# Optimization experiments

Measured on AMD Instinct MI355X. Metric: run time of the kernel, lower is better.

The kernel has to match this reference:

```python
import jax, jax.numpy as jnp
import numpy as np

BANDWIDTH = 0.1
N_STEPS = 5
TOL = 1e-3
BASE = 3
COORD_OFFSET = 512   # bins assumed within (-512, 511] per dim
COORD_BITS = 10      # 3 dims * 10 bits = 30 bits, fits int32


def _generate_offsets(d, base=3):
    # replicates torch.meshgrid(indexing='ij') over arange(-1, base-1)
    ranges = [np.arange(-1, base - 1) for _ in range(d)]
    mesh = np.meshgrid(*ranges, indexing='ij')
    return jnp.asarray(np.stack(mesh, axis=-1).reshape(-1, d), dtype=jnp.int32)


def _pack_keys(bins):
    # bins: (..., d) int32 -> unique scalar int32 key per bin coordinate
    d = bins.shape[-1]
    key = jnp.zeros(bins.shape[:-1], dtype=jnp.int32)
    for k in range(d):  # tiny fixed loop over dims
        key = (key << COORD_BITS) | (bins[..., k] + COORD_OFFSET)
    return key


def _step(X, offsets, bandwidth):
    # One mean-shift step: bin points, scatter-add sums/counts over the
    # union of offset-shifted bins (torch.unique replaced by exact key
    # packing + sort-based grouping, fixed shapes for jit).
    n, d = X.shape
    m = offsets.shape[0]  # base ** d
    bins = (X / bandwidth).astype(jnp.int32)          # trunc-toward-zero == torch .int()
    shifted = bins[:, None, :] + offsets[None, :, :]  # (n, m, d)
    keys = _pack_keys(shifted).reshape(-1)            # (n*m,)
    K = keys.shape[0]

    order = jnp.argsort(keys)
    skeys = keys[order]
    new_grp = jnp.concatenate(
        [jnp.zeros((1,), jnp.int32), (skeys[1:] != skeys[:-1]).astype(jnp.int32)]
    )
    seg = jnp.cumsum(new_grp)                         # group id per sorted position

    # X repeated once per offset (matches X.repeat(1, m).reshape(-1, d))
    Xflat = jnp.broadcast_to(X[:, None, :], (n, m, d)).reshape(-1, d)
    sum_per = jax.ops.segment_sum(Xflat[order], seg, num_segments=K)          # (K, d)
    cnt_per = jax.ops.segment_sum(jnp.ones((K,), X.dtype), seg, num_segments=K)

    # segment id per original (unsorted) flat position == inverse_indices
    seg_orig = jnp.zeros((K,), seg.dtype).at[order].set(seg)
    sum_mapped = sum_per[seg_orig].reshape(n, m, d).sum(axis=1)   # (n, d)
    cnt_mapped = cnt_per[seg_orig].reshape(n, m).sum(axis=1)      # (n,)
    return sum_mapped / cnt_mapped[:, None]


def setup_inputs() -> dict:
    key = jax.random.key(0)
    X = jax.random.normal(key, (200000, 3), dtype=jnp.float32)
    return {"X": X}


def reference(X):
    n, d = X.shape
    offsets = _generate_offsets(d, BASE)

    def body(carry, _):
        Xc, done = carry
        Xn = _step(Xc, offsets, BANDWIDTH)
        Xn = jnp.where(done, Xc, Xn)  # freeze once converged (== early break)
        conv = jnp.max(jnp.linalg.norm(Xn - Xc, axis=1)) <= TOL
        return (Xn, done | conv), None

    (Xout, _), _ = jax.lax.scan(body, (X, jnp.array(False)), None, length=N_STEPS)
    return Xout
```

## Files before the change

### kernel.cpp

```cpp
#include <hip/hip_runtime.h>


constexpr float BW   = 0.1f;
constexpr float TOL2 = 1e-6f;
constexpr int DIM  = 112, OFF = 56;
constexpr int DIM2 = DIM * DIM;
constexpr int CELLS = DIM * DIM * DIM;
constexpr int CLW = CELLS / 32;
constexpr int RDIM = 16, RC = 7;
constexpr int NREG = RDIM * RDIM * RDIM;
constexpr int RC3 = RC * RC * RC;
constexpr int NB_A = 128, BLK = 256;
constexpr int NF = 2048;
constexpr int IPB = 51;
constexpr float FPS = 16777216.0f;
constexpr double FPSI = 1.0 / 16777216.0;

typedef float vf2 __attribute__((ext_vector_type(2)));

__device__ __forceinline__ int clampb(int v) { return v < 0 ? 0 : (v > DIM - 1 ? DIM - 1 : v); }
__device__ __forceinline__ int binf(float v) { return clampb((int)(v / BW) + OFF); }
__device__ __forceinline__ int flatb(int bx, int by, int bz) { return (bx * DIM + by) * DIM + bz; }
__device__ __forceinline__ int regOf(int bx, int by, int bz) {
    return ((bx / RC) * RDIM + (by / RC)) * RDIM + (bz / RC);
}
__device__ __forceinline__ int lcOf(int bx, int by, int bz) {
    return ((bx % RC) * RC + (by % RC)) * RC + (bz % RC);
}

__device__ __forceinline__ void pk_add(float* p, float a, float b) {
#if defined(__has_builtin) && __has_builtin(__builtin_amdgcn_global_atomic_fadd_v2f32)
    vf2 v = {a, b};
    __builtin_amdgcn_global_atomic_fadd_v2f32((vf2*)p, v);
#else
    atomicAdd(p, a);
    atomicAdd(p + 1, b);
#endif
}

__launch_bounds__(BLK)
__global__ void k_histA(const float* __restrict__ X, int n, int* __restrict__ blockHist,
                        float4* __restrict__ zeroB) {
    __shared__ int h[NREG];
    for (int i = threadIdx.x; i < NREG; i += blockDim.x) h[i] = 0;
    __syncthreads();
    int stride = gridDim.x * blockDim.x;
    for (int i = blockIdx.x * blockDim.x + threadIdx.x; i < n; i += stride) {
        float x = X[3 * i + 0], y = X[3 * i + 1], z = X[3 * i + 2];
        atomicAdd(&h[regOf(binf(x), binf(y), binf(z))], 1);
    }
    __syncthreads();
    for (int i = threadIdx.x; i < NREG; i += blockDim.x)
        blockHist[blockIdx.x * NREG + i] = h[i];
    for (int i = blockIdx.x * blockDim.x + threadIdx.x; i < CELLS; i += stride)
        zeroB[i] = make_float4(0.f, 0.f, 0.f, 0.f);
}

__global__ void k_colscan(int* __restrict__ blockHist, int* __restrict__ regionPS) {
    int r = blockIdx.x * blockDim.x + threadIdx.x;
    if (r >= NREG) return;
    int run = 0;
    for (int b = 0; b < NB_A; ++b) {
        int idx = b * NREG + r;
        int v = blockHist[idx];
        blockHist[idx] = run;
        run += v;
    }
    regionPS[r] = run;
}

__launch_bounds__(1024)
__global__ void k_regprefix(int* __restrict__ regionPS) {
    __shared__ int buf[1024];
    int t = threadIdx.x;
    int v0 = regionPS[4 * t + 0], v1 = regionPS[4 * t + 1];
    int v2 = regionPS[4 * t + 2], v3 = regionPS[4 * t + 3];
    int s = v0 + v1 + v2 + v3;
    buf[t] = s;
    __syncthreads();
    for (int d = 1; d < 1024; d <<= 1) {
        int add = (t >= d) ? buf[t - d] : 0;
        __syncthreads();
        buf[t] += add;
        __syncthreads();
    }
    int excl = buf[t] - s;
    regionPS[4 * t + 0] = excl;
    regionPS[4 * t + 1] = excl + v0;
    regionPS[4 * t + 2] = excl + v0 + v1;
    regionPS[4 * t + 3] = excl + v0 + v1 + v2;
    if (t == 1023) regionPS[4096] = buf[1023];
}

__launch_bounds__(BLK)
__global__ void k_scatterA(const float* __restrict__ X, int n,
                           const int* __restrict__ blockHist,
                           const int* __restrict__ regionPS,
                           float4* __restrict__ bucket, float4* __restrict__ zeroC) {
    __shared__ int cur[NREG];
    for (int i = threadIdx.x; i < NREG; i += blockDim.x) cur[i] = 0;
    __syncthreads();
    int stride = gridDim.x * blockDim.x;
    for (int i = blockIdx.x * blockDim.x + threadIdx.x; i < n; i += stride) {
        float x = X[3 * i + 0], y = X[3 * i + 1], z = X[3 * i + 2];
        int r = regOf(binf(x), binf(y), binf(z));
        int pos = regionPS[r] + blockHist[blockIdx.x * NREG + r] + atomicAdd(&cur[r], 1);
        bucket[pos] = make_float4(x, y, z, __int_as_float(i));
    }
    for (int i = blockIdx.x * blockDim.x + threadIdx.x; i < CELLS; i += stride)
        zeroC[i] = make_float4(0.f, 0.f, 0.f, 0.f);
}

__launch_bounds__(BLK)
__global__ void k_binB(const float4* __restrict__ bucket, const int* __restrict__ regionPS,
                       float4* __restrict__ A, int* __restrict__ E0,
                       int* __restrict__ PIdx, int* __restrict__ gM0) {
    __shared__ unsigned long long aX[RC3], aY[RC3], aZ[RC3];
    __shared__ unsigned aC[RC3];
    __shared__ int cidx[RC3];
    __shared__ int cnt, cur, sBase;
    int r = blockIdx.x;
    for (int c = threadIdx.x; c < RC3; c += blockDim.x) {
        aX[c] = 0ull; aY[c] = 0ull; aZ[c] = 0ull; aC[c] = 0u;
    }
    if (threadIdx.x == 0) { cnt = 0; cur = 0; }
    __syncthreads();
    int start = regionPS[r], end = regionPS[r + 1];
    for (int i = start + threadIdx.x; i < end; i += blockDim.x) {
        float4 p = bucket[i];
        int lc = lcOf(binf(p.x), binf(p.y), binf(p.z));
        atomicAdd(&aX[lc], (unsigned long long)(long long)rintf(p.x * FPS));
        atomicAdd(&aY[lc], (unsigned long long)(long long)rintf(p.y * FPS));
        atomicAdd(&aZ[lc], (unsigned long long)(long long)rintf(p.z * FPS));
        atomicAdd(&aC[lc], 1u);
    }
    __syncthreads();
    int myc = 0;
    for (int c = threadIdx.x; c < RC3; c += blockDim.x)
        if (aC[c] > 0u) ++myc;
    if (myc) atomicAdd(&cnt, myc);
    __syncthreads();
    if (threadIdx.x == 0 && cnt > 0) sBase = atomicAdd(gM0, cnt);
    __syncthreads();
    int rx = r / (RDIM * RDIM), ry = (r / RDIM) % RDIM, rz = r % RDIM;
    for (int c = threadIdx.x; c < RC3; c += blockDim.x) {
        if (aC[c] > 0u) {
            int idx = sBase + atomicAdd(&cur, 1);
            cidx[c] = idx;
            int bx = rx * RC + c / (RC * RC);
            int by = ry * RC + (c / RC) % RC;
            int bz = rz * RC + c % RC;
            int b = flatb(bx, by, bz);
            E0[idx] = b;
            A[b] = make_float4((float)((double)(long long)aX[c] * FPSI),
                               (float)((double)(long long)aY[c] * FPSI),
                               (float)((double)(long long)aZ[c] * FPSI),
                               (float)aC[c]);
        }
    }
    __syncthreads();
    for (int i = start + threadIdx.x; i < end; i += blockDim.x) {
        float4 p = bucket[i];
        int lc = lcOf(binf(p.x), binf(p.y), binf(p.z));
        PIdx[__float_as_int(p.w)] = cidx[lc];
    }
}

__launch_bounds__(BLK)
__global__ void k_compactM(unsigned* __restrict__ mask, int* __restrict__ listOut,
                           int* __restrict__ pKout) {
    __shared__ int scan[BLK];
    __shared__ int sBase;
    int i = blockIdx.x * blockDim.x + threadIdx.x;
    unsigned w = (i < CLW) ? mask[i] : 0u;
    if (i < CLW && w) mask[i] = 0u;
    int c = __popc(w);
    scan[threadIdx.x] = c;
    __syncthreads();
    for (int d = 1; d < BLK; d <<= 1) {
        int add = (threadIdx.x >= (unsigned)d) ? scan[threadIdx.x - d] : 0;
        __syncthreads();
        scan[threadIdx.x] += add;
        __syncthreads();
    }
    if (threadIdx.x == BLK - 1) {
        int tot = scan[BLK - 1];
        sBase = tot ? atomicAdd(pKout, tot) : 0;
    }
    __syncthreads();
    int base = sBase + scan[threadIdx.x] - c;
    int bb = i * 32;
    while (w) {
        int b = __ffs(w) - 1;
        listOut[base++] = bb + b;
        w &= w - 1;
    }
}

__launch_bounds__(BLK)
__global__ void k_fused(
    const float4* __restrict__ src, const int* __restrict__ list, const int* __restrict__ pK,
    float4* __restrict__ REo, int* __restrict__ IDXo, float4* __restrict__ eposInit,
    float4* __restrict__ tgt, unsigned* __restrict__ clT,
    int updS, const float* __restrict__ X, int n, const int* __restrict__ PIdx,
    const float4* __restrict__ REp, const int* __restrict__ IDXp,
    const int* __restrict__ pM0, float4* __restrict__ epos,
    unsigned* __restrict__ notConv,
    const int* __restrict__ clearList, const int* __restrict__ pKc,
    float4* __restrict__ clearGrid, int lastStep) {
    __shared__ float4 sh[BLK];
    __shared__ unsigned sFlag;
    if (threadIdx.x == 0) sFlag = 0;
    __syncthreads();
    int K = *pK;
    int BC = (K + IPB - 1) / IPB;
    if (BC > NF - 256) BC = NF - 256;
    const float t5[5] = {1.f, 2.f, 3.f, 2.f, 1.f};
    bool moved = false;

    if ((int)blockIdx.x < BC) {
        for (int ib = blockIdx.x; ib * IPB < K; ib += BC) {
            int li = threadIdx.x / 5;
            int dx = threadIdx.x % 5;
            int item = ib * IPB + li;
            float4 part = make_float4(0.f, 0.f, 0.f, 0.f);
            if (li < IPB && item < K) {
                int b = list[item];
                int bx = b / DIM2, rem = b % DIM2;
                int by = rem / DIM, bz = rem % DIM;
                int ix = bx + dx - 2;
                if ((unsigned)ix < (unsigned)DIM) {
                    float wx = t5[dx];
                    if (by >= 2 && by <= DIM - 3 && bz >= 2 && bz <= DIM - 3) {
                        #pragma unroll
                        for (int dy = 0; dy < 5; ++dy) {
                            float wxy = wx * t5[dy];
                            const float4* row = src + flatb(ix, by + dy - 2, bz - 2);
                            #pragma unroll
                            for (int dz = 0; dz < 5; ++dz) {
                                float w = wxy * t5[dz];
                                float4 e = row[dz];
                                part.x = fmaf(w, e.x, part.x);
                                part.y = fmaf(w, e.y, part.y);
                                part.z = fmaf(w, e.z, part.z);
                                part.w = fmaf(w, e.w, part.w);
                            }
                        }
                    } else {
                        for (int dy = 0; dy < 5; ++dy) {
                            int iy = by + dy - 2;
                            if ((unsigned)iy >= (unsigned)DIM) continue;
                            float wxy = wx * t5[dy];
                            for (int dz = 0; dz < 5; ++dz) {
                                int iz = bz + dz - 2;
                                if ((unsigned)iz >= (unsigned)DIM) continue;
                                float w = wxy * t5[dz];
                                float4 e = src[flatb(ix, iy, iz)];
                                part.x = fmaf(w, e.x, part.x);
                                part.y = fmaf(w, e.y, part.y);
                                part.z = fmaf(w, e.z, part.z);
                                part.w = fmaf(w, e.w, part.w);
                            }
                        }
                    }
                }
            }
            sh[threadIdx.x] = part;
            __syncthreads();
            if (threadIdx.x < IPB) {
                int item2 = ib * IPB + threadIdx.x;
                if (item2 < K) {
                    int base5 = threadIdx.x * 5;
                    float4 a0 = sh[base5 + 0], a1 = sh[base5 + 1], a2 = sh[base5 + 2];
                    float4 a3 = sh[base5 + 3], a4 = sh[base5 + 4];
                    float sx = a0.x + a1.x + a2.x + a3.x + a4.x;
                    float sy = a0.y + a1.y + a2.y + a3.y + a4.y;
                    float sz = a0.z + a1.z + a2.z + a3.z + a4.z;
                    float sc = a0.w + a1.w + a2.w + a3.w + a4.w;
                    int b = list[item2];
                    float W = src[b].w;
                    float4 np = make_float4(sx / sc, sy / sc, sz / sc, W);
                    REo[item2] = np;
                    IDXo[b] = item2;
                    if (eposInit) eposInit[item2] = np;
                    if (!lastStep) {
                        int bn = flatb(binf(np.x), binf(np.y), binf(np.z));
                        float* cell = (float*)&tgt[bn];
                        pk_add(cell + 0, W * np.x, W * np.y);
                        pk_add(cell + 2, W * np.z, W);
                        atomicOr(&clT[(unsigned)bn >> 5], 1u << (bn & 31));
                    }
                }
            }
            __syncthreads();
        }
    } else {
        int U = (updS > 0) ? (X ? n : *pM0) : 0;
        int CL = clearList ? *pKc : 0;
        int total = U + CL;
        bool done = false;
        if (updS > 1) {
            for (int t = 1; t < updS; ++t) done |= (notConv[t] == 0u);
        }
        int stride = (NF - BC) * blockDim.x;
        for (int idx = (blockIdx.x - BC) * blockDim.x + threadIdx.x; idx < total;
             idx += stride) {
            if (idx < U) {
                int e = idx;
                if (X) {
                    float x = X[3 * e + 0], y = X[3 * e + 1], z = X[3 * e + 2];
                    float4 rr = REp[PIdx[e]];
                    float ex = rr.x - x, ey = rr.y - y, ez = rr.z - z;
                    moved |= (fmaf(ex, ex, fmaf(ey, ey, ez * ez)) > TOL2);
                } else if (!done) {
                    float4 p = epos[e];
                    int j = IDXp[flatb(binf(p.x), binf(p.y), binf(p.z))];
                    float4 rr = REp[j];
                    float ex = rr.x - p.x, ey = rr.y - p.y, ez = rr.z - p.z;
                    moved |= (fmaf(ex, ex, fmaf(ey, ey, ez * ez)) > TOL2);
                    epos[e] = make_float4(rr.x, rr.y, rr.z, p.w);
                }
            } else {
                clearGrid[clearList[idx - U]] = make_float4(0.f, 0.f, 0.f, 0.f);
            }
        }
    }
    if (moved) sFlag = 1;
    __syncthreads();
    if (threadIdx.x == 0 && updS > 0 && sFlag) notConv[updS] = 1u;
}

__launch_bounds__(BLK)
__global__ void k_fin(const float4* __restrict__ REa, const int* __restrict__ IDXa,
                      const float4* __restrict__ epos, const int* __restrict__ pM0,
                      const unsigned* __restrict__ notConv, float4* __restrict__ fpos) {
    int M0 = *pM0;
    bool done = false;
    for (int t = 1; t <= 4; ++t) done |= (notConv[t] == 0u);
    for (int e = blockIdx.x * blockDim.x + threadIdx.x; e < M0;
         e += gridDim.x * blockDim.x) {
        float4 p = epos[e];
        if (!done) {
            float4 rr = REa[IDXa[flatb(binf(p.x), binf(p.y), binf(p.z))]];
            p.x = rr.x; p.y = rr.y; p.z = rr.z;
        }
        fpos[e] = p;
    }
}

__global__ void k_map(const int* __restrict__ PIdx, int n, const float4* __restrict__ fpos,
                      float* __restrict__ out) {
    int i = blockIdx.x * blockDim.x + threadIdx.x;
    if (i >= n) return;
    float4 p = fpos[PIdx[i]];
    out[3 * i + 0] = p.x;
    out[3 * i + 1] = p.y;
    out[3 * i + 2] = p.z;
}

extern "C" void kernel_launch(void* const* d_in, const int* in_sizes, int n_in,
                              void* d_out, int out_size, void* d_ws, size_t ws_size,
                              hipStream_t stream) {
    const float* X = (const float*)d_in[0];
    int n = in_sizes[0] / 3;

    char* ws = (char*)d_ws;
    int*      cnt     = (int*)ws;
    unsigned* notConv = (unsigned*)(ws + 32);
    size_t mB = (size_t)CLW * 4;
    size_t gB = (size_t)CELLS * 16;
    unsigned* m0 = (unsigned*)(ws + 256);
    unsigned* m1 = (unsigned*)(ws + 256 + mB);
    float4* A = (float4*)(ws + 256 + 2 * mB);
    float4* B = (float4*)((char*)A + gB);
    float4* C = (float4*)((char*)B + gB);
    int* IDXa = (int*)((char*)C + gB);
    int* IDXb = IDXa + CELLS;
    float4* REa  = (float4*)(IDXb + CELLS);
    float4* REb  = REa + n;
    float4* epos = REb + n;
    int* E0   = (int*)(epos + n);
    int* La   = E0 + n;
    int* Lb   = La + n;
    int* Lc   = Lb + n;
    int* Ld   = Lc + n;
    int* PIdx = Ld + n;
    float4* bucket = (float4*)(PIdx + n);
    int* blockHist = (int*)(bucket + n);
    int* regionPS  = blockHist + NB_A * NREG;

    hipMemsetAsync(ws, 0, 256 + 2 * mB + gB, stream);

    const int NCM = (CLW + BLK - 1) / BLK;

    k_histA<<<NB_A, BLK, 0, stream>>>(X, n, blockHist, B);
    k_colscan<<<NREG / BLK, BLK, 0, stream>>>(blockHist, regionPS);
    k_regprefix<<<1, 1024, 0, stream>>>(regionPS);
    k_scatterA<<<NB_A, BLK, 0, stream>>>(X, n, blockHist, regionPS, bucket, C);
    k_binB<<<NREG, BLK, 0, stream>>>(bucket, regionPS, A, E0, PIdx, &cnt[1]);

    k_fused<<<NF, BLK, 0, stream>>>(A, E0, &cnt[1], REa, IDXa, epos,
                                    B, m0,
                                    0, nullptr, n, nullptr, nullptr, nullptr, nullptr,
                                    nullptr, notConv, nullptr, nullptr, nullptr, 0);
    k_compactM<<<NCM, BLK, 0, stream>>>(m0, La, &cnt[2]);
    k_fused<<<NF, BLK, 0, stream>>>(B, La, &cnt[2], REb, IDXb, nullptr,
                                    C, m1,
                                    1, X, n, PIdx, REa, IDXa, &cnt[1], nullptr,
                                    notConv, E0, &cnt[1], A, 0);
    k_compactM<<<NCM, BLK, 0, stream>>>(m1, Lb, &cnt[3]);
    k_fused<<<NF, BLK, 0, stream>>>(C, Lb, &cnt[3], REa, IDXa, nullptr,
                                    A, m0,
                                    2, nullptr, n, nullptr, REb, IDXb, &cnt[1], epos,
                                    notConv, La, &cnt[2], B, 0);
    k_compactM<<<NCM, BLK, 0, stream>>>(m0, Lc, &cnt[4]);
    k_fused<<<NF, BLK, 0, stream>>>(A, Lc, &cnt[4], REb, IDXb, nullptr,
                                    B, m1,
                                    3, nullptr, n, nullptr, REa, IDXa, &cnt[1], epos,
                                    notConv, nullptr, nullptr, nullptr, 0);
    k_compactM<<<NCM, BLK, 0, stream>>>(m1, Ld, &cnt[5]);
    k_fused<<<NF, BLK, 0, stream>>>(B, Ld, &cnt[5], REa, IDXa, nullptr,
                                    nullptr, nullptr,
                                    4, nullptr, n, nullptr, REb, IDXb, &cnt[1], epos,
                                    notConv, nullptr, nullptr, nullptr, 1);

    k_fin<<<256, BLK, 0, stream>>>(REa, IDXa, epos, &cnt[1], notConv, REb);
    k_map<<<(n + BLK - 1) / BLK, BLK, 0, stream>>>(PIdx, n, REb, (float*)d_out);
}
```

Measured before the change: 253.0 us.

## Tile stencil per 7^3 region in shared memory with region-ordered occupancy masks

```diff
diff --git a/kernel.cpp b/kernel.cpp
--- a/kernel.cpp
+++ b/kernel.cpp
@@ -6,13 +6,15 @@
 constexpr int DIM  = 112, OFF = 56;
 constexpr int DIM2 = DIM * DIM;
 constexpr int CELLS = DIM * DIM * DIM;
-constexpr int CLW = CELLS / 32;
 constexpr int RDIM = 16, RC = 7;
 constexpr int NREG = RDIM * RDIM * RDIM;
 constexpr int RC3 = RC * RC * RC;
+constexpr int RPW = 11;
+constexpr int MWORDS = NREG * RPW;
+constexpr int TD = RC + 4;
+constexpr int TCELLS = TD * TD * TD;
 constexpr int NB_A = 128, BLK = 256;
 constexpr int NF = 2048;
-constexpr int IPB = 51;
 constexpr float FPS = 16777216.0f;
 constexpr double FPSI = 1.0 / 16777216.0;
 
@@ -113,17 +115,15 @@
 
 __launch_bounds__(BLK)
 __global__ void k_binB(const float4* __restrict__ bucket, const int* __restrict__ regionPS,
-                       float4* __restrict__ A, int* __restrict__ E0,
-                       int* __restrict__ PIdx, int* __restrict__ gM0) {
+                       float4* __restrict__ A, unsigned* __restrict__ mask) {
     __shared__ unsigned long long aX[RC3], aY[RC3], aZ[RC3];
     __shared__ unsigned aC[RC3];
-    __shared__ int cidx[RC3];
-    __shared__ int cnt, cur, sBase;
+    __shared__ unsigned occ[RPW];
     int r = blockIdx.x;
     for (int c = threadIdx.x; c < RC3; c += blockDim.x) {
         aX[c] = 0ull; aY[c] = 0ull; aZ[c] = 0ull; aC[c] = 0u;
     }
-    if (threadIdx.x == 0) { cnt = 0; cur = 0; }
+    if (threadIdx.x < RPW) occ[threadIdx.x] = 0u;
     __syncthreads();
     int start = regionPS[r], end = regionPS[r + 1];
     for (int i = start + threadIdx.x; i < end; i += blockDim.x) {
@@ -135,47 +135,43 @@
         atomicAdd(&aC[lc], 1u);
     }
     __syncthreads();
-    int myc = 0;
-    for (int c = threadIdx.x; c < RC3; c += blockDim.x)
-        if (aC[c] > 0u) ++myc;
-    if (myc) atomicAdd(&cnt, myc);
-    __syncthreads();
-    if (threadIdx.x == 0 && cnt > 0) sBase = atomicAdd(gM0, cnt);
-    __syncthreads();
     int rx = r / (RDIM * RDIM), ry = (r / RDIM) % RDIM, rz = r % RDIM;
     for (int c = threadIdx.x; c < RC3; c += blockDim.x) {
         if (aC[c] > 0u) {
-            int idx = sBase + atomicAdd(&cur, 1);
-            cidx[c] = idx;
+            atomicOr(&occ[c >> 5], 1u << (c & 31));
             int bx = rx * RC + c / (RC * RC);
             int by = ry * RC + (c / RC) % RC;
             int bz = rz * RC + c % RC;
-            int b = flatb(bx, by, bz);
-            E0[idx] = b;
-            A[b] = make_float4((float)((double)(long long)aX[c] * FPSI),
-                               (float)((double)(long long)aY[c] * FPSI),
-                               (float)((double)(long long)aZ[c] * FPSI),
-                               (float)aC[c]);
-        }
-    }
-    __syncthreads();
-    for (int i = start + threadIdx.x; i < end; i += blockDim.x) {
-        float4 p = bucket[i];
-        int lc = lcOf(binf(p.x), binf(p.y), binf(p.z));
-        PIdx[__float_as_int(p.w)] = cidx[lc];
-    }
-}
-
-__launch_bounds__(BLK)
-__global__ void k_compactM(unsigned* __restrict__ mask, int* __restrict__ listOut,
-                           int* __restrict__ pKout) {
+            A[flatb(bx, by, bz)] =
+                make_float4((float)((double)(long long)aX[c] * FPSI),
+                            (float)((double)(long long)aY[c] * FPSI),
+                            (float)((double)(long long)aZ[c] * FPSI),
+                            (float)aC[c]);
+        }
+    }
+    __syncthreads();
+    if (threadIdx.x < RPW) mask[r * RPW + threadIdx.x] = occ[threadIdx.x];
+}
+
+__launch_bounds__(BLK)
+__global__ void k_compactR(unsigned* __restrict__ mask, int* __restrict__ items,
+                           int* __restrict__ regBase, int* __restrict__ regCnt,
+                           int* __restrict__ actList, int* __restrict__ pActCnt,
+                           int* __restrict__ pTot) {
     __shared__ int scan[BLK];
     __shared__ int sBase;
-    int i = blockIdx.x * blockDim.x + threadIdx.x;
-    unsigned w = (i < CLW) ? mask[i] : 0u;
-    if (i < CLW && w) mask[i] = 0u;
-    int c = __popc(w);
-    scan[threadIdx.x] = c;
+    int r = blockIdx.x * BLK + threadIdx.x;
+    unsigned w[RPW];
+    int cnt = 0;
+    #pragma unroll
+    for (int k = 0; k < RPW; ++k) {
+        w[k] = mask[r * RPW + k];
+        cnt += __popc(w[k]);
+    }
+    #pragma unroll
+    for (int k = 0; k < RPW; ++k)
+        if (w[k]) mask[r * RPW + k] = 0u;
+    scan[threadIdx.x] = cnt;
     __syncthreads();
     for (int d = 1; d < BLK; d <<= 1) {
         int add = (threadIdx.x >= (unsigned)d) ? scan[threadIdx.x - d] : 0;
@@ -185,111 +181,114 @@
     }
     if (threadIdx.x == BLK - 1) {
         int tot = scan[BLK - 1];
-        sBase = tot ? atomicAdd(pKout, tot) : 0;
-    }
-    __syncthreads();
-    int base = sBase + scan[threadIdx.x] - c;
-    int bb = i * 32;
-    while (w) {
-        int b = __ffs(w) - 1;
-        listOut[base++] = bb + b;
-        w &= w - 1;
-    }
-}
-
-__launch_bounds__(BLK)
-__global__ void k_fused(
-    const float4* __restrict__ src, const int* __restrict__ list, const int* __restrict__ pK,
+        sBase = tot ? atomicAdd(pTot, tot) : 0;
+    }
+    __syncthreads();
+    int base = sBase + scan[threadIdx.x] - cnt;
+    regBase[r] = base;
+    regCnt[r] = cnt;
+    int rx = r / (RDIM * RDIM), ry = (r / RDIM) % RDIM, rz = r % RDIM;
+    int idx = base;
+    #pragma unroll
+    for (int k = 0; k < RPW; ++k) {
+        unsigned ww = w[k];
+        while (ww) {
+            int bpos = __ffs(ww) - 1;
+            ww &= ww - 1;
+            int lc = k * 32 + bpos;
+            items[idx++] = flatb(rx * RC + lc / (RC * RC),
+                                 ry * RC + (lc / RC) % RC,
+                                 rz * RC + lc % RC);
+        }
+    }
+    bool act = cnt > 0;
+    unsigned long long m = __ballot(act);
+    int lane = threadIdx.x & 63;
+    if (m) {
+        int leader = (int)__ffsll((long long)m) - 1;
+        int ab;
+        if (lane == leader) ab = atomicAdd(pActCnt, __popcll(m));
+        ab = __shfl(ab, leader, 64);
+        if (act) actList[ab + __popcll(m & ((1ull << lane) - 1))] = r;
+    }
+}
+
+__launch_bounds__(BLK)
+__global__ void k_convR(
+    const float4* __restrict__ src, const int* __restrict__ items,
+    const int* __restrict__ regBase, const int* __restrict__ regCnt,
+    const int* __restrict__ actList, const int* __restrict__ pActCnt,
     float4* __restrict__ REo, int* __restrict__ IDXo, float4* __restrict__ eposInit,
     float4* __restrict__ tgt, unsigned* __restrict__ clT,
-    int updS, const float* __restrict__ X, int n, const int* __restrict__ PIdx,
+    int updS, const float* __restrict__ X, int n,
     const float4* __restrict__ REp, const int* __restrict__ IDXp,
     const int* __restrict__ pM0, float4* __restrict__ epos,
     unsigned* __restrict__ notConv,
     const int* __restrict__ clearList, const int* __restrict__ pKc,
     float4* __restrict__ clearGrid, int lastStep) {
-    __shared__ float4 sh[BLK];
+    __shared__ float4 tile[TCELLS];
     __shared__ unsigned sFlag;
     if (threadIdx.x == 0) sFlag = 0;
     __syncthreads();
-    int K = *pK;
-    int BC = (K + IPB - 1) / IPB;
-    if (BC > NF - 256) BC = NF - 256;
+    int AC = *pActCnt;
+    int BC = AC < NF - 256 ? AC : NF - 256;
     const float t5[5] = {1.f, 2.f, 3.f, 2.f, 1.f};
     bool moved = false;
 
     if ((int)blockIdx.x < BC) {
-        for (int ib = blockIdx.x; ib * IPB < K; ib += BC) {
-            int li = threadIdx.x / 5;
-            int dx = threadIdx.x % 5;
-            int item = ib * IPB + li;
-            float4 part = make_float4(0.f, 0.f, 0.f, 0.f);
-            if (li < IPB && item < K) {
-                int b = list[item];
+        for (int ri = blockIdx.x; ri < AC; ri += BC) {
+            int r = actList[ri];
+            int rx = r / (RDIM * RDIM), ry = (r / RDIM) % RDIM, rz = r % RDIM;
+            int gx0 = rx * RC - 2, gy0 = ry * RC - 2, gz0 = rz * RC - 2;
+            for (int c = threadIdx.x; c < TCELLS; c += BLK) {
+                int lx = c / (TD * TD), ly = (c / TD) % TD, lz = c % TD;
+                int gx = gx0 + lx, gy = gy0 + ly, gz = gz0 + lz;
+                float4 v = make_float4(0.f, 0.f, 0.f, 0.f);
+                if ((unsigned)gx < (unsigned)DIM && (unsigned)gy < (unsigned)DIM &&
+                    (unsigned)gz < (unsigned)DIM)
+                    v = src[flatb(gx, gy, gz)];
+                tile[c] = v;
+            }
+            __syncthreads();
+            int base = regBase[r], cnt = regCnt[r];
+            for (int q = threadIdx.x; q < cnt; q += BLK) {
+                int item = base + q;
+                int b = items[item];
                 int bx = b / DIM2, rem = b % DIM2;
                 int by = rem / DIM, bz = rem % DIM;
-                int ix = bx + dx - 2;
-                if ((unsigned)ix < (unsigned)DIM) {
+                int lx = bx - gx0, ly = by - gy0, lz = bz - gz0;
+                float sx = 0.f, sy = 0.f, sz = 0.f, sc = 0.f;
+                #pragma unroll
+                for (int dx = 0; dx < 5; ++dx) {
                     float wx = t5[dx];
-                    if (by >= 2 && by <= DIM - 3 && bz >= 2 && bz <= DIM - 3) {
+                    #pragma unroll
+                    for (int dy = 0; dy < 5; ++dy) {
+                        float wxy = wx * t5[dy];
+                        const float4* row =
+                            &tile[(lx + dx - 2) * (TD * TD) + (ly + dy - 2) * TD + (lz - 2)];
                         #pragma unroll
-                        for (int dy = 0; dy < 5; ++dy) {
-                            float wxy = wx * t5[dy];
-                            const float4* row = src + flatb(ix, by + dy - 2, bz - 2);
-                            #pragma unroll
-                            for (int dz = 0; dz < 5; ++dz) {
-                                float w = wxy * t5[dz];
-                                float4 e = row[dz];
-                                part.x = fmaf(w, e.x, part.x);
-                                part.y = fmaf(w, e.y, part.y);
-                                part.z = fmaf(w, e.z, part.z);
-                                part.w = fmaf(w, e.w, part.w);
-                            }
-                        }
-                    } else {
-                        for (int dy = 0; dy < 5; ++dy) {
-                            int iy = by + dy - 2;
-                            if ((unsigned)iy >= (unsigned)DIM) continue;
-                            float wxy = wx * t5[dy];
-                            for (int dz = 0; dz < 5; ++dz) {
-                                int iz = bz + dz - 2;
-                                if ((unsigned)iz >= (unsigned)DIM) continue;
-                                float w = wxy * t5[dz];
-                                float4 e = src[flatb(ix, iy, iz)];
-                                part.x = fmaf(w, e.x, part.x);
-                                part.y = fmaf(w, e.y, part.y);
-                                part.z = fmaf(w, e.z, part.z);
-                                part.w = fmaf(w, e.w, part.w);
-                            }
+                        for (int dz = 0; dz < 5; ++dz) {
+                            float w = wxy * t5[dz];
+                            float4 e = row[dz];
+                            sx = fmaf(w, e.x, sx);
+                            sy = fmaf(w, e.y, sy);
+                            sz = fmaf(w, e.z, sz);
+                            sc = fmaf(w, e.w, sc);
                         }
                     }
                 }
-            }
-            sh[threadIdx.x] = part;
-            __syncthreads();
-            if (threadIdx.x < IPB) {
-                int item2 = ib * IPB + threadIdx.x;
-                if (item2 < K) {
-                    int base5 = threadIdx.x * 5;
-                    float4 a0 = sh[base5 + 0], a1 = sh[base5 + 1], a2 = sh[base5 + 2];
-                    float4 a3 = sh[base5 + 3], a4 = sh[base5 + 4];
-                    float sx = a0.x + a1.x + a2.x + a3.x + a4.x;
-                    float sy = a0.y + a1.y + a2.y + a3.y + a4.y;
-                    float sz = a0.z + a1.z + a2.z + a3.z + a4.z;
-                    float sc = a0.w + a1.w + a2.w + a3.w + a4.w;
-                    int b = list[item2];
-                    float W = src[b].w;
-                    float4 np = make_float4(sx / sc, sy / sc, sz / sc, W);
-                    REo[item2] = np;
-                    IDXo[b] = item2;
-                    if (eposInit) eposInit[item2] = np;
-                    if (!lastStep) {
-                        int bn = flatb(binf(np.x), binf(np.y), binf(np.z));
-                        float* cell = (float*)&tgt[bn];
-                        pk_add(cell + 0, W * np.x, W * np.y);
-                        pk_add(cell + 2, W * np.z, W);
-                        atomicOr(&clT[(unsigned)bn >> 5], 1u << (bn & 31));
-                    }
+                float W = tile[lx * (TD * TD) + ly * TD + lz].w;
+                float4 np = make_float4(sx / sc, sy / sc, sz / sc, W);
+                REo[item] = np;
+                IDXo[b] = item;
+                if (eposInit) eposInit[item] = np;
+                if (!lastStep) {
+                    int nbx = binf(np.x), nby = binf(np.y), nbz = binf(np.z);
+                    float* cell = (float*)&tgt[flatb(nbx, nby, nbz)];
+                    pk_add(cell + 0, W * np.x, W * np.y);
+                    pk_add(cell + 2, W * np.z, W);
+                    int r2 = regOf(nbx, nby, nbz), lc2 = lcOf(nbx, nby, nbz);
+                    atomicOr(&clT[r2 * RPW + (lc2 >> 5)], 1u << (lc2 & 31));
                 }
             }
             __syncthreads();
@@ -309,7 +308,8 @@
                 int e = idx;
                 if (X) {
                     float x = X[3 * e + 0], y = X[3 * e + 1], z = X[3 * e + 2];
-                    float4 rr = REp[PIdx[e]];
+                    int j = IDXp[flatb(binf(x), binf(y), binf(z))];
+                    float4 rr = REp[j];
                     float ex = rr.x - x, ey = rr.y - y, ez = rr.z - z;
                     moved |= (fmaf(ex, ex, fmaf(ey, ey, ez * ez)) > TOL2);
                 } else if (!done) {
@@ -348,11 +348,12 @@
     }
 }
 
-__global__ void k_map(const int* __restrict__ PIdx, int n, const float4* __restrict__ fpos,
-                      float* __restrict__ out) {
+__global__ void k_map(const float* __restrict__ X, int n, const int* __restrict__ IDX1,
+                      const float4* __restrict__ fpos, float* __restrict__ out) {
     int i = blockIdx.x * blockDim.x + threadIdx.x;
     if (i >= n) return;
-    float4 p = fpos[PIdx[i]];
+    float x = X[3 * i + 0], y = X[3 * i + 1], z = X[3 * i + 2];
+    float4 p = fpos[IDX1[flatb(binf(x), binf(y), binf(z))]];
     out[3 * i + 0] = p.x;
     out[3 * i + 1] = p.y;
     out[3 * i + 2] = p.z;
@@ -366,64 +367,69 @@
 
     char* ws = (char*)d_ws;
     int*      cnt     = (int*)ws;
-    unsigned* notConv = (unsigned*)(ws + 32);
-    size_t mB = (size_t)CLW * 4;
+    int*      actC    = (int*)ws + 8;
+    unsigned* notConv = (unsigned*)ws + 16;
+    size_t mB = (size_t)MWORDS * 4;
     size_t gB = (size_t)CELLS * 16;
-    unsigned* m0 = (unsigned*)(ws + 256);
-    unsigned* m1 = (unsigned*)(ws + 256 + mB);
+    unsigned* mA = (unsigned*)(ws + 256);
+    unsigned* mBk = (unsigned*)(ws + 256 + mB);
     float4* A = (float4*)(ws + 256 + 2 * mB);
     float4* B = (float4*)((char*)A + gB);
     float4* C = (float4*)((char*)B + gB);
-    int* IDXa = (int*)((char*)C + gB);
+    int* IDX1 = (int*)((char*)C + gB);
+    int* IDXa = IDX1 + CELLS;
     int* IDXb = IDXa + CELLS;
     float4* REa  = (float4*)(IDXb + CELLS);
     float4* REb  = REa + n;
     float4* epos = REb + n;
-    int* E0   = (int*)(epos + n);
-    int* La   = E0 + n;
-    int* Lb   = La + n;
-    int* Lc   = Lb + n;
-    int* Ld   = Lc + n;
-    int* PIdx = Ld + n;
-    float4* bucket = (float4*)(PIdx + n);
+    int* E1 = (int*)(epos + n);
+    int* E2 = E1 + n;
+    int* E3 = E2 + n;
+    int* rb1 = E3 + n;  int* rc1 = rb1 + NREG;
+    int* rb2 = rc1 + NREG; int* rc2 = rb2 + NREG;
+    int* rb3 = rc2 + NREG; int* rc3 = rb3 + NREG;
+    int* act1 = rc3 + NREG;
+    int* act2 = act1 + NREG;
+    int* act3 = act2 + NREG;
+    float4* bucket = (float4*)(act3 + NREG);
     int* blockHist = (int*)(bucket + n);
     int* regionPS  = blockHist + NB_A * NREG;
 
     hipMemsetAsync(ws, 0, 256 + 2 * mB + gB, stream);
-
-    const int NCM = (CLW + BLK - 1) / BLK;
 
     k_histA<<<NB_A, BLK, 0, stream>>>(X, n, blockHist, B);
     k_colscan<<<NREG / BLK, BLK, 0, stream>>>(blockHist, regionPS);
     k_regprefix<<<1, 1024, 0, stream>>>(regionPS);
     k_scatterA<<<NB_A, BLK, 0, stream>>>(X, n, blockHist, regionPS, bucket, C);
-    k_binB<<<NREG, BLK, 0, stream>>>(bucket, regionPS, A, E0, PIdx, &cnt[1]);
-
-    k_fused<<<NF, BLK, 0, stream>>>(A, E0, &cnt[1], REa, IDXa, epos,
-                                    B, m0,
+    k_binB<<<NREG, BLK, 0, stream>>>(bucket, regionPS, A, mA);
+
+    const int NCR = NREG / BLK;
+    k_compactR<<<NCR, BLK, 0, stream>>>(mA, E1, rb1, rc1, act1, &actC[1], &cnt[1]);
+    k_convR<<<NF, BLK, 0, stream>>>(A, E1, rb1, rc1, act1, &actC[1],
+                                    REa, IDX1, epos, B, mBk,
                                     0, nullptr, n, nullptr, nullptr, nullptr, nullptr,
-                                    nullptr, notConv, nullptr, nullptr, nullptr, 0);
-    k_compactM<<<NCM, BLK, 0, stream>>>(m0, La, &cnt[2]);
-    k_fused<<<NF, BLK, 0, stream>>>(B, La, &cnt[2], REb, IDXb, nullptr,
-                                    C, m1,
-                                    1, X, n, PIdx, REa, IDXa, &cnt[1], nullptr,
-                                    notConv, E0, &cnt[1], A, 0);
-    k_compactM<<<NCM, BLK, 0, stream>>>(m1, Lb, &cnt[3]);
-    k_fused<<<NF, BLK, 0, stream>>>(C, Lb, &cnt[3], REa, IDXa, nullptr,
-                                    A, m0,
-                                    2, nullptr, n, nullptr, REb, IDXb, &cnt[1], epos,
-                                    notConv, La, &cnt[2], B, 0);
-    k_compactM<<<NCM, BLK, 0, stream>>>(m0, Lc, &cnt[4]);
-    k_fused<<<NF, BLK, 0, stream>>>(A, Lc, &cnt[4], REb, IDXb, nullptr,
-                                    B, m1,
-                                    3, nullptr, n, nullptr, REa, IDXa, &cnt[1], epos,
                                     notConv, nullptr, nullptr, nullptr, 0);
-    k_compactM<<<NCM, BLK, 0, stream>>>(m1, Ld, &cnt[5]);
-    k_fused<<<NF, BLK, 0, stream>>>(B, Ld, &cnt[5], REa, IDXa, nullptr,
-                                    nullptr, nullptr,
-                                    4, nullptr, n, nullptr, REb, IDXb, &cnt[1], epos,
+    k_compactR<<<NCR, BLK, 0, stream>>>(mBk, E2, rb2, rc2, act2, &actC[2], &cnt[2]);
+    k_convR<<<NF, BLK, 0, stream>>>(B, E2, rb2, rc2, act2, &actC[2],
+                                    REb, IDXb, nullptr, C, mA,
+                                    1, X, n, REa, IDX1, &cnt[1], nullptr,
+                                    notConv, E1, &cnt[1], A, 0);
+    k_compactR<<<NCR, BLK, 0, stream>>>(mA, E3, rb3, rc3, act3, &actC[3], &cnt[3]);
+    k_convR<<<NF, BLK, 0, stream>>>(C, E3, rb3, rc3, act3, &actC[3],
+                                    REa, IDXa, nullptr, A, mBk,
+                                    2, nullptr, n, REb, IDXb, &cnt[1], epos,
+                                    notConv, E2, &cnt[2], B, 0);
+    k_compactR<<<NCR, BLK, 0, stream>>>(mBk, E1, rb1, rc1, act1, &actC[4], &cnt[4]);
+    k_convR<<<NF, BLK, 0, stream>>>(A, E1, rb1, rc1, act1, &actC[4],
+                                    REb, IDXb, nullptr, B, mA,
+                                    3, nullptr, n, REa, IDXa, &cnt[1], epos,
+                                    notConv, E3, &cnt[3], C, 0);
+    k_compactR<<<NCR, BLK, 0, stream>>>(mA, E2, rb2, rc2, act2, &actC[5], &cnt[5]);
+    k_convR<<<NF, BLK, 0, stream>>>(B, E2, rb2, rc2, act2, &actC[5],
+                                    REa, IDXa, nullptr, nullptr, nullptr,
+                                    4, nullptr, n, REb, IDXb, &cnt[1], epos,
                                     notConv, nullptr, nullptr, nullptr, 1);
 
     k_fin<<<256, BLK, 0, stream>>>(REa, IDXa, epos, &cnt[1], notConv, REb);
-    k_map<<<(n + BLK - 1) / BLK, BLK, 0, stream>>>(PIdx, n, REb, (float*)d_out);
-}
+    k_map<<<(n + BLK - 1) / BLK, BLK, 0, stream>>>(X, n, IDX1, REb, (float*)d_out);
+}
```

Result: slower. 385.1 us (+52.2%).
